# Optimization experiments

Measured on AMD Instinct MI355X. Metric: run time of the kernel, lower is better.

The kernel has to match this reference:

```python
import jax, jax.numpy as jnp
import numpy as np

QW_MAX = 127  # 2**(8-1) - 1


def setup_inputs() -> dict:
    key = jax.random.key(0)
    k1, k2, k3, k4, k5 = jax.random.split(key, 5)
    B, Din, H, Dout = 4096, 1024, 4096, 1024
    x = jax.random.normal(k1, (B, Din), dtype=jnp.float32)
    # float master weights (already transposed, as in quantify_weights: weight.T)
    w1f = jax.random.normal(k2, (Din, H), dtype=jnp.float32) * 0.02
    b1f = jax.random.normal(k3, (H,), dtype=jnp.float32) * 0.02
    w2f = jax.random.normal(k4, (H, Dout), dtype=jnp.float32) * 0.02
    b2f = jax.random.normal(k5, (Dout,), dtype=jnp.float32) * 0.02
    return {"x": x, "w1f": w1f, "b1f": b1f, "w2f": w2f, "b2f": b2f}


def _quantify_pair(w, b):
    # joint max-abs scale over weight and bias (matches quantify(x, x2))
    max_v = jnp.maximum(jnp.max(jnp.abs(w)), jnp.max(jnp.abs(b)))
    scale = max_v / QW_MAX
    wq = jnp.round(w / scale).astype(jnp.int8)
    bq = jnp.round(b / scale).astype(jnp.int8)
    return wq, bq, scale


def _dot_product(q_a, q_b, scale_a, scale_b, target_scale):
    # int8 GEMM with int32 accumulation, then requantize to int16
    y0 = q_a.astype(jnp.int32) @ q_b.astype(jnp.int32)  # [M, N] int32
    scale = scale_a * scale_b / target_scale
    return jnp.round(y0 * scale).astype(jnp.int16)


def reference(x, w1f, b1f, w2f, b2f):
    # weight quantization (done once at init in torch, inlined here)
    w1, b1, s1 = _quantify_pair(w1f, b1f)
    w2, b2, s2 = _quantify_pair(w2f, b2f)
    # dynamic activation quantization
    x_scale = jnp.max(jnp.abs(x)) / QW_MAX
    x_q = jnp.round(x / x_scale).astype(jnp.int8)
    # layer 1: target_scale = s1, so effective multiplier is x_scale
    o1 = _dot_product(x_q, w1, x_scale, s1, s1) + b1.astype(jnp.int16)
    # layer 2: note torch passes scale_1 (not x_scale) here — faithful to source
    o2 = _dot_product(jnp.maximum(o1, 0), w2, s1, s2, s2) + b2.astype(jnp.int16)
    # dequantize
    return o2.astype(jnp.float32) * s2
```

## Files before the change

kernel.cpp:

```cpp
#include <hip/hip_runtime.h>
#include <stdint.h>

typedef int   i32x4 __attribute__((ext_vector_type(4)));
typedef float f32x4 __attribute__((ext_vector_type(4)));

#define WS_PART    0
#define WS_XQ      32768
#define WS_W1QT    (WS_XQ   + 4096*1024)
#define WS_W2QT    (WS_W1QT + 4096*1024)
#define WS_PS      (WS_W2QT + 4096*1024)
#define WS_PH      (WS_PS   + 4096*4096)

__device__ __forceinline__ void async16(const void* g, void* l) {
  __builtin_amdgcn_global_load_lds(
      (const __attribute__((address_space(1))) unsigned*)g,
      (__attribute__((address_space(3))) unsigned*)l, 16, 0, 0);
}

__device__ __forceinline__ float block_absmax(const float* __restrict__ p0, int n0,
                                              const float* __restrict__ p1, int n1,
                                              float* red, float* slot) {
  int tid = threadIdx.x, nt = blockDim.x;
  float m = 0.f;
  for (int i = tid; i < n0; i += nt) m = fmaxf(m, fabsf(p0[i]));
  if (p1) for (int i = tid; i < n1; i += nt) m = fmaxf(m, fabsf(p1[i]));
  for (int off = 32; off; off >>= 1) m = fmaxf(m, __shfl_down(m, off));
  if ((tid & 63) == 0) red[tid >> 6] = m;
  __syncthreads();
  if (tid == 0) {
    int nw = nt >> 6;
    float M = red[0];
    for (int w = 1; w < nw; w++) M = fmaxf(M, red[w]);
    *slot = M;
  }
  __syncthreads();
  return *slot;
}

__global__ void k_absmax3(const float* __restrict__ x, const float* __restrict__ w1,
                          const float* __restrict__ w2, float* __restrict__ part) {
  int seg = blockIdx.x >> 9;
  int b = blockIdx.x & 511;
  const float* p = (seg == 0) ? x : (seg == 1) ? w1 : w2;
  int i = b * 256 + threadIdx.x;
  float m = 0.f;
  #pragma unroll
  for (int it = 0; it < 8; it++) {
    f32x4 v = ((const f32x4*)p)[i + it * 131072];
    m = fmaxf(m, fmaxf(fmaxf(fabsf(v.x), fabsf(v.y)), fmaxf(fabsf(v.z), fabsf(v.w))));
  }
  for (int off = 32; off; off >>= 1) m = fmaxf(m, __shfl_down(m, off));
  __shared__ float red[4];
  if ((threadIdx.x & 63) == 0) red[threadIdx.x >> 6] = m;
  __syncthreads();
  if (threadIdx.x == 0)
    part[blockIdx.x] = fmaxf(fmaxf(red[0], red[1]), fmaxf(red[2], red[3]));
}

__device__ __forceinline__ void quantT_body(const float* __restrict__ w, float s,
                                            i32x4* __restrict__ out, int C, int tkbits,
                                            int b) {
  int L = b * 256 + threadIdx.x;
  int h_in = L & 127;
  int kb = (L >> 7) & 3;
  int tk = (L >> 9) & ((1 << tkbits) - 1);
  int hblk = L >> (9 + tkbits);
  int h = hblk * 128 + h_in;
  int k0 = (tk * 4 + kb) * 16;
  int wd[4];
  #pragma unroll
  for (int d = 0; d < 4; d++) {
    unsigned acc = 0;
    #pragma unroll
    for (int j = 0; j < 4; j++) {
      float v = w[(size_t)(k0 + d * 4 + j) * C + h];
      int q = (int)rintf(v / s) & 255;
      acc |= (unsigned)q << (8 * j);
    }
    wd[d] = (int)acc;
  }
  i32x4 o; o.x = wd[0]; o.y = wd[1]; o.z = wd[2]; o.w = wd[3];
  out[L] = o;
}

__global__ void k_prep(const float* __restrict__ x, const float* __restrict__ w1f,
                       const float* __restrict__ w2f, const float* __restrict__ b1f,
                       const float* __restrict__ b2f, const float* __restrict__ part,
                       i32x4* __restrict__ xq, i32x4* __restrict__ w1qt,
                       i32x4* __restrict__ w2qt) {
  __shared__ float red[4];
  __shared__ float slot;
  int seg = blockIdx.x >> 10;
  int b = blockIdx.x & 1023;
  if (seg == 0) {
    float s = block_absmax(part, 512, nullptr, 0, red, &slot) / 127.0f;
    int L = b * 256 + threadIdx.x;
    int m_in = L & 127, kb = (L >> 7) & 3, tk = (L >> 9) & 15, mblk = L >> 13;
    int m = mblk * 128 + m_in;
    int k0 = (tk * 4 + kb) * 16;
    const f32x4* px = (const f32x4*)(x + m * 1024 + k0);
    int wd[4];
    #pragma unroll
    for (int d = 0; d < 4; d++) {
      f32x4 v = px[d];
      int b0 = (int)rintf(v.x / s) & 255;
      int b1 = (int)rintf(v.y / s) & 255;
      int b2 = (int)rintf(v.z / s) & 255;
      int b3 = (int)rintf(v.w / s) & 255;
      wd[d] = b0 | (b1 << 8) | (b2 << 16) | (b3 << 24);
    }
    i32x4 o; o.x = wd[0]; o.y = wd[1]; o.z = wd[2]; o.w = wd[3];
    xq[L] = o;
  } else if (seg == 1) {
    float s = block_absmax(part + 512, 512, b1f, 4096, red, &slot) / 127.0f;
    quantT_body(w1f, s, w1qt, 4096, 4, b);
  } else {
    float s = block_absmax(part + 1024, 512, b2f, 1024, red, &slot) / 127.0f;
    quantT_body(w2f, s, w2qt, 1024, 6, b);
  }
}

__launch_bounds__(256)
__global__ void k_gemm1(const i32x4* __restrict__ Aq, const i32x4* __restrict__ Bq,
                        const float* __restrict__ part, const float* __restrict__ b1f,
                        unsigned* __restrict__ plane_s, unsigned* __restrict__ plane_h) {
  __shared__ i32x4 As[2][512];
  __shared__ i32x4 Bs[2][512];
  __shared__ float red[4];
  __shared__ float slot;
  __shared__ int b1s[128];
  int tid = threadIdx.x;
  int bb = blockIdx.x;
  int hb = blockIdx.y;
  int lane = tid & 63, wid = tid >> 6;
  int wm = wid & 1, wn = wid >> 1;
  int g = lane >> 4, l15 = lane & 15;

  const i32x4* gA = Aq + (size_t)hb * 16 * 512;
  const i32x4* gB = Bq + (size_t)bb * 16 * 512;

  async16(gA + tid, &As[0][tid]);
  async16(gA + tid + 256, &As[0][tid + 256]);
  async16(gB + tid, &Bs[0][tid]);
  async16(gB + tid + 256, &Bs[0][tid + 256]);

  float sx  = block_absmax(part, 512, nullptr, 0, red, &slot) / 127.0f;
  float s1v = block_absmax(part + 512, 512, b1f, 4096, red, &slot) / 127.0f;
  float mult1 = sx * s1v / s1v;
  for (int i = tid; i < 128; i += 256)
    b1s[i] = (int)rintf(b1f[hb * 128 + i] / s1v);

  i32x4 acc[4][4];
  #pragma unroll
  for (int r = 0; r < 4; r++)
    #pragma unroll
    for (int c = 0; c < 4; c++) acc[r][c] = (i32x4)(0);

  int abase = g * 128 + wm * 64 + l15;
  int bbase = g * 128 + wn * 64 + l15;

  for (int t = 0; t < 16; ++t) {
    int cur = t & 1;
    __syncthreads();
    if (t + 1 < 16) {
      const i32x4* ga = gA + (t + 1) * 512;
      const i32x4* gb = gB + (t + 1) * 512;
      async16(ga + tid, &As[cur ^ 1][tid]);
      async16(ga + tid + 256, &As[cur ^ 1][tid + 256]);
      async16(gb + tid, &Bs[cur ^ 1][tid]);
      async16(gb + tid + 256, &Bs[cur ^ 1][tid + 256]);
    }
    i32x4 af[4], bf[4];
    #pragma unroll
    for (int r = 0; r < 4; r++) af[r] = As[cur][abase + r * 16];
    #pragma unroll
    for (int c = 0; c < 4; c++) bf[c] = Bs[cur][bbase + c * 16];
    #pragma unroll
    for (int r = 0; r < 4; r++)
      #pragma unroll
      for (int c = 0; c < 4; c++)
        acc[r][c] = __builtin_amdgcn_mfma_i32_16x16x64_i8(af[r], bf[c], acc[r][c], 0, 0, 0);
  }

  int t2base = hb * 2 + wm;
  #pragma unroll
  for (int r = 0; r < 4; r++) {
    int hloc = wm * 64 + r * 16 + 4 * g;
    int bq0 = b1s[hloc], bq1 = b1s[hloc + 1], bq2 = b1s[hloc + 2], bq3 = b1s[hloc + 3];
    #pragma unroll
    for (int c = 0; c < 4; c++) {
      unsigned lo = 0, hi = 0;
      #pragma unroll
      for (int q = 0; q < 4; q++) {
        int y0 = acc[r][c][q];
        int bqv = (q == 0) ? bq0 : (q == 1) ? bq1 : (q == 2) ? bq2 : bq3;
        int o = (short)((int)rintf((float)y0 * mult1) + bqv);
        int a = o > 0 ? o : 0;
        int s8 = (int)(signed char)(a & 0xFF);
        int h8 = (a >> 8) + (s8 < 0 ? 1 : 0);
        lo |= (unsigned)(s8 & 0xFF) << (8 * q);
        hi |= (unsigned)(h8 & 0xFF) << (8 * q);
      }
      int m_in = wn * 64 + c * 16 + l15;
      unsigned idx = (((unsigned)(bb * 64 + t2base) * 512u + (unsigned)(r * 128 + m_in)) << 2) + g;
      plane_s[idx] = lo;
      plane_h[idx] = hi;
    }
  }
}

__launch_bounds__(512)
__global__ void k_gemm2(const i32x4* __restrict__ Ps, const i32x4* __restrict__ Ph,
                        const i32x4* __restrict__ Bq, const float* __restrict__ part,
                        const float* __restrict__ b1f, const float* __restrict__ b2f,
                        float* __restrict__ out) {
  __shared__ i32x4 st[3][1536];
  __shared__ float red[8];
  __shared__ float slot;

  int tid = threadIdx.x;
  int bid = blockIdx.x;
  int wg  = (bid & 7) * 32 + (bid >> 3);
  int mb = wg >> 3;
  int nb = wg & 7;
  int wid = tid >> 6, lane = tid & 63;
  int wm = wid >> 1;
  int wn = wid & 1;
  int g = lane >> 4, l15 = lane & 15;

  size_t mbase = (size_t)mb * 64;
  size_t nbase = (size_t)nb * 64;

  #pragma unroll
  for (int tt = 0; tt < 2; ++tt) {
    const i32x4* pS = Ps + ((mbase + tt) << 9);
    const i32x4* pH = Ph + ((mbase + tt) << 9);
    const i32x4* pB = Bq + ((nbase + tt) << 9);
    async16(pS + tid, &st[tt][tid]);
    async16(pH + tid, &st[tt][512 + tid]);
    async16(pB + tid, &st[tt][1024 + tid]);
  }

  float s1v = block_absmax(part + 512, 512, b1f, 4096, red, &slot) / 127.0f;
  float s2v = block_absmax(part + 1024, 512, b2f, 1024, red, &slot) / 127.0f;
  float mult2 = s1v * s2v / s2v;
  int bq[4];
  #pragma unroll
  for (int c = 0; c < 4; c++)
    bq[c] = (int)rintf(b2f[nb * 128 + wn * 64 + c * 16 + l15] / s2v);

  i32x4 accS[2][4], accH[2][4];
  #pragma unroll
  for (int r = 0; r < 2; r++)
    #pragma unroll
    for (int c = 0; c < 4; c++) { accS[r][c] = (i32x4)(0); accH[r][c] = (i32x4)(0); }

  int aoff = g * 128 + wm * 32 + l15;
  int boff = 1024 + g * 128 + wn * 64 + l15;

  int cb = 0;
  for (int t = 0; t < 64; ++t) {
    int pb = cb + 2; if (pb >= 3) pb -= 3;
    if (t + 2 < 64) {
      const i32x4* pS = Ps + ((mbase + t + 2) << 9);
      const i32x4* pH = Ph + ((mbase + t + 2) << 9);
      async16(pS + tid, &st[pb][tid]);
      async16(pH + tid, &st[pb][512 + tid]);
    }
    i32x4 aS0 = st[cb][aoff];
    i32x4 aH0 = st[cb][512 + aoff];
    i32x4 bf[4];
    #pragma unroll
    for (int c = 0; c < 4; c++) bf[c] = st[cb][boff + c * 16];
    __builtin_amdgcn_s_barrier();
    __builtin_amdgcn_s_setprio(1);
    #pragma unroll
    for (int c = 0; c < 4; c++) {
      accS[0][c] = __builtin_amdgcn_mfma_i32_16x16x64_i8(aS0, bf[c], accS[0][c], 0, 0, 0);
      accH[0][c] = __builtin_amdgcn_mfma_i32_16x16x64_i8(aH0, bf[c], accH[0][c], 0, 0, 0);
    }
    __builtin_amdgcn_s_setprio(0);
    __builtin_amdgcn_s_barrier();
    if (t + 2 < 64) {
      const i32x4* pB = Bq + ((nbase + t + 2) << 9);
      async16(pB + tid, &st[pb][1024 + tid]);
    }
    i32x4 aS1 = st[cb][aoff + 16];
    i32x4 aH1 = st[cb][512 + aoff + 16];
    __builtin_amdgcn_s_barrier();
    __builtin_amdgcn_s_setprio(1);
    #pragma unroll
    for (int c = 0; c < 4; c++) {
      accS[1][c] = __builtin_amdgcn_mfma_i32_16x16x64_i8(aS1, bf[c], accS[1][c], 0, 0, 0);
      accH[1][c] = __builtin_amdgcn_mfma_i32_16x16x64_i8(aH1, bf[c], accH[1][c], 0, 0, 0);
    }
    __builtin_amdgcn_s_setprio(0);
    if (t < 62) asm volatile("s_waitcnt vmcnt(3)");
    else        asm volatile("s_waitcnt vmcnt(0)");
    __builtin_amdgcn_s_barrier();
    __builtin_amdgcn_sched_barrier(0);
    cb = cb + 1; if (cb >= 3) cb -= 3;
  }

  #pragma unroll
  for (int r = 0; r < 2; r++) {
    int m0 = mb * 128 + wm * 32 + r * 16 + 4 * g;
    #pragma unroll
    for (int c = 0; c < 4; c++) {
      int n = nb * 128 + wn * 64 + c * 16 + l15;
      #pragma unroll
      for (int q = 0; q < 4; q++) {
        int y0 = accS[r][c][q] + accH[r][c][q] * 256;
        int o = (short)((int)rintf((float)y0 * mult2) + bq[c]);
        out[(size_t)(m0 + q) * 1024 + n] = (float)o * s2v;
      }
    }
  }
}

extern "C" void kernel_launch(void* const* d_in, const int* in_sizes, int n_in,
                              void* d_out, int out_size, void* d_ws, size_t ws_size,
                              hipStream_t stream) {
  const float* x   = (const float*)d_in[0];
  const float* w1f = (const float*)d_in[1];
  const float* b1f = (const float*)d_in[2];
  const float* w2f = (const float*)d_in[3];
  const float* b2f = (const float*)d_in[4];
  float* out = (float*)d_out;

  char* ws = (char*)d_ws;
  float*  part    = (float*)(ws + WS_PART);
  i32x4*  xq      = (i32x4*)(ws + WS_XQ);
  i32x4*  w1qt    = (i32x4*)(ws + WS_W1QT);
  i32x4*  w2qt    = (i32x4*)(ws + WS_W2QT);
  unsigned* ps    = (unsigned*)(ws + WS_PS);
  unsigned* ph    = (unsigned*)(ws + WS_PH);

  k_absmax3<<<1536, 256, 0, stream>>>(x, w1f, w2f, part);
  k_prep<<<3072, 256, 0, stream>>>(x, w1f, w2f, b1f, b2f, part, xq, w1qt, w2qt);
  k_gemm1<<<dim3(32, 32), 256, 0, stream>>>(w1qt, xq, part, b1f, ps, ph);
  k_gemm2<<<256, 512, 0, stream>>>((const i32x4*)ps, (const i32x4*)ph, w2qt,
                                   part, b1f, b2f, out);
}
```

Before: 184.6 us.

## Halve gemm2 M-tile to 64 rows with 256-thread blocks and 512 workgroups

Splits each 128x128 output tile of the second GEMM into two 64-row halves, launching 512 blocks of 256 threads instead of 256 blocks of 512. Each block loads half of the A planes (selected by a_src) plus the full B tile, and the inner loop drops the split-phase barriers so all 16 MFMAs issue in one group per k-step. This is meant to raise occupancy and CU coverage (256 blocks underfill the GPU) at the cost of loading B twice and reduced reuse per block.

```diff
diff --git a/kernel.cpp b/kernel.cpp
--- a/kernel.cpp
+++ b/kernel.cpp
@@ -209,45 +209,46 @@
   }
 }
 
-__launch_bounds__(512)
+__launch_bounds__(256)
 __global__ void k_gemm2(const i32x4* __restrict__ Ps, const i32x4* __restrict__ Ph,
                         const i32x4* __restrict__ Bq, const float* __restrict__ part,
                         const float* __restrict__ b1f, const float* __restrict__ b2f,
                         float* __restrict__ out) {
-  __shared__ i32x4 st[3][1536];
-  __shared__ float red[8];
+  __shared__ i32x4 st[3][1024];
+  __shared__ float red[4];
   __shared__ float slot;
 
   int tid = threadIdx.x;
   int bid = blockIdx.x;
-  int wg  = (bid & 7) * 32 + (bid >> 3);
+  int wg  = (bid & 7) * 64 + (bid >> 3);
   int mb = wg >> 3;
   int nb = wg & 7;
+  int mblk = mb >> 1, half = mb & 1;
   int wid = tid >> 6, lane = tid & 63;
-  int wm = wid >> 1;
-  int wn = wid & 1;
+  int wm = wid >> 1, wn = wid & 1;
   int g = lane >> 4, l15 = lane & 15;
 
-  size_t mbase = (size_t)mb * 64;
-  size_t nbase = (size_t)nb * 64;
+  int a_src = wid * 128 + half * 64 + lane;
+  int a_dst = wid * 64 + lane;
 
   #pragma unroll
   for (int tt = 0; tt < 2; ++tt) {
-    const i32x4* pS = Ps + ((mbase + tt) << 9);
-    const i32x4* pH = Ph + ((mbase + tt) << 9);
-    const i32x4* pB = Bq + ((nbase + tt) << 9);
-    async16(pS + tid, &st[tt][tid]);
-    async16(pH + tid, &st[tt][512 + tid]);
-    async16(pB + tid, &st[tt][1024 + tid]);
+    const i32x4* pS = Ps + ((size_t)(mblk * 64 + tt) << 9);
+    const i32x4* pH = Ph + ((size_t)(mblk * 64 + tt) << 9);
+    const i32x4* pB = Bq + ((size_t)(nb * 64 + tt) << 9);
+    async16(pS + a_src, &st[tt][a_dst]);
+    async16(pH + a_src, &st[tt][256 + a_dst]);
+    async16(pB + tid,       &st[tt][512 + tid]);
+    async16(pB + tid + 256, &st[tt][768 + tid]);
   }
 
   float s1v = block_absmax(part + 512, 512, b1f, 4096, red, &slot) / 127.0f;
   float s2v = block_absmax(part + 1024, 512, b2f, 1024, red, &slot) / 127.0f;
   float mult2 = s1v * s2v / s2v;
-  int bq[4];
+  int bq4[4];
   #pragma unroll
   for (int c = 0; c < 4; c++)
-    bq[c] = (int)rintf(b2f[nb * 128 + wn * 64 + c * 16 + l15] / s2v);
+    bq4[c] = (int)rintf(b2f[nb * 128 + wn * 64 + c * 16 + l15] / s2v);
 
   i32x4 accS[2][4], accH[2][4];
   #pragma unroll
@@ -255,47 +256,39 @@
     #pragma unroll
     for (int c = 0; c < 4; c++) { accS[r][c] = (i32x4)(0); accH[r][c] = (i32x4)(0); }
 
-  int aoff = g * 128 + wm * 32 + l15;
-  int boff = 1024 + g * 128 + wn * 64 + l15;
+  int aoff = g * 64 + wm * 32 + l15;
+  int boff = 512 + g * 128 + wn * 64 + l15;
 
   int cb = 0;
   for (int t = 0; t < 64; ++t) {
-    int pb = cb + 2; if (pb >= 3) pb -= 3;
     if (t + 2 < 64) {
-      const i32x4* pS = Ps + ((mbase + t + 2) << 9);
-      const i32x4* pH = Ph + ((mbase + t + 2) << 9);
-      async16(pS + tid, &st[pb][tid]);
-      async16(pH + tid, &st[pb][512 + tid]);
-    }
-    i32x4 aS0 = st[cb][aoff];
-    i32x4 aH0 = st[cb][512 + aoff];
-    i32x4 bf[4];
+      int pb = cb + 2; if (pb >= 3) pb -= 3;
+      const i32x4* pS = Ps + ((size_t)(mblk * 64 + t + 2) << 9);
+      const i32x4* pH = Ph + ((size_t)(mblk * 64 + t + 2) << 9);
+      const i32x4* pB = Bq + ((size_t)(nb * 64 + t + 2) << 9);
+      async16(pS + a_src, &st[pb][a_dst]);
+      async16(pH + a_src, &st[pb][256 + a_dst]);
+      async16(pB + tid,       &st[pb][512 + tid]);
+      async16(pB + tid + 256, &st[pb][768 + tid]);
+    }
+    i32x4 aS[2], aH[2], bf[4];
+    #pragma unroll
+    for (int r = 0; r < 2; r++) {
+      aS[r] = st[cb][aoff + r * 16];
+      aH[r] = st[cb][256 + aoff + r * 16];
+    }
     #pragma unroll
     for (int c = 0; c < 4; c++) bf[c] = st[cb][boff + c * 16];
-    __builtin_amdgcn_s_barrier();
     __builtin_amdgcn_s_setprio(1);
     #pragma unroll
-    for (int c = 0; c < 4; c++) {
-      accS[0][c] = __builtin_amdgcn_mfma_i32_16x16x64_i8(aS0, bf[c], accS[0][c], 0, 0, 0);
-      accH[0][c] = __builtin_amdgcn_mfma_i32_16x16x64_i8(aH0, bf[c], accH[0][c], 0, 0, 0);
-    }
+    for (int r = 0; r < 2; r++)
+      #pragma unroll
+      for (int c = 0; c < 4; c++) {
+        accS[r][c] = __builtin_amdgcn_mfma_i32_16x16x64_i8(aS[r], bf[c], accS[r][c], 0, 0, 0);
+        accH[r][c] = __builtin_amdgcn_mfma_i32_16x16x64_i8(aH[r], bf[c], accH[r][c], 0, 0, 0);
+      }
     __builtin_amdgcn_s_setprio(0);
-    __builtin_amdgcn_s_barrier();
-    if (t + 2 < 64) {
-      const i32x4* pB = Bq + ((nbase + t + 2) << 9);
-      async16(pB + tid, &st[pb][1024 + tid]);
-    }
-    i32x4 aS1 = st[cb][aoff + 16];
-    i32x4 aH1 = st[cb][512 + aoff + 16];
-    __builtin_amdgcn_s_barrier();
-    __builtin_amdgcn_s_setprio(1);
-    #pragma unroll
-    for (int c = 0; c < 4; c++) {
-      accS[1][c] = __builtin_amdgcn_mfma_i32_16x16x64_i8(aS1, bf[c], accS[1][c], 0, 0, 0);
-      accH[1][c] = __builtin_amdgcn_mfma_i32_16x16x64_i8(aH1, bf[c], accH[1][c], 0, 0, 0);
-    }
-    __builtin_amdgcn_s_setprio(0);
-    if (t < 62) asm volatile("s_waitcnt vmcnt(3)");
+    if (t < 62) asm volatile("s_waitcnt vmcnt(4)");
     else        asm volatile("s_waitcnt vmcnt(0)");
     __builtin_amdgcn_s_barrier();
     __builtin_amdgcn_sched_barrier(0);
@@ -304,14 +297,14 @@
 
   #pragma unroll
   for (int r = 0; r < 2; r++) {
-    int m0 = mb * 128 + wm * 32 + r * 16 + 4 * g;
+    int m0 = mb * 64 + wm * 32 + r * 16 + 4 * g;
     #pragma unroll
     for (int c = 0; c < 4; c++) {
       int n = nb * 128 + wn * 64 + c * 16 + l15;
       #pragma unroll
       for (int q = 0; q < 4; q++) {
         int y0 = accS[r][c][q] + accH[r][c][q] * 256;
-        int o = (short)((int)rintf((float)y0 * mult2) + bq[c]);
+        int o = (short)((int)rintf((float)y0 * mult2) + bq4[c]);
         out[(size_t)(m0 + q) * 1024 + n] = (float)o * s2v;
       }
     }
@@ -339,6 +332,6 @@
   k_absmax3<<<1536, 256, 0, stream>>>(x, w1f, w2f, part);
   k_prep<<<3072, 256, 0, stream>>>(x, w1f, w2f, b1f, b2f, part, xq, w1qt, w2qt);
   k_gemm1<<<dim3(32, 32), 256, 0, stream>>>(w1qt, xq, part, b1f, ps, ph);
-  k_gemm2<<<256, 512, 0, stream>>>((const i32x4*)ps, (const i32x4*)ph, w2qt,
+  k_gemm2<<<512, 256, 0, stream>>>((const i32x4*)ps, (const i32x4*)ph, w2qt,
                                    part, b1f, b2f, out);
 }
```

Result: slower. 192.0 us (+4.0%).
